# Kernel optimization log

Hardware: AMD Instinct MI355X
Metric: run time of the kernel (lower is better)

The kernel has to match this reference:

```python
import jax, jax.numpy as jnp
import numpy as np

H, W = 480, 640
N = 256
CFEAT = 256
FAR = 80.0

def _quat_to_rot(q):
    # q: [N,4] normalized (w,x,y,z)
    w, x, y, z = q[:, 0], q[:, 1], q[:, 2], q[:, 3]
    return jnp.stack([
        jnp.stack([1 - 2 * (y * y + z * z), 2 * (x * y - w * z), 2 * (x * z + w * y)], -1),
        jnp.stack([2 * (x * y + w * z), 1 - 2 * (x * x + z * z), 2 * (y * z - w * x)], -1),
        jnp.stack([2 * (x * z - w * y), 2 * (y * z + w * x), 1 - 2 * (x * x + y * y)], -1)], -2)

def setup_inputs():
    key = jax.random.key(0)
    ks = jax.random.split(key, 10)
    z = jax.random.uniform(ks[0], (N,), minval=2.0, maxval=30.0)
    x = jax.random.uniform(ks[1], (N,), minval=-0.6, maxval=0.6) * z
    y = jax.random.uniform(ks[2], (N,), minval=-0.45, maxval=0.45) * z
    means3d = jnp.stack([x, y, z], -1)                                   # [N,3] in front of camera
    features = jax.random.normal(ks[3], (N, CFEAT))                      # [N,256]
    opacities = jax.random.uniform(ks[4], (N,), minval=0.3, maxval=0.95)
    scales = jax.random.uniform(ks[5], (N, 3), minval=0.05, maxval=0.4)
    rotations = jax.random.normal(ks[6], (N, 4))                         # unnormalized quats
    cam_K = jnp.array([[500.0, 0.0, 320.0], [0.0, 500.0, 240.0], [0.0, 0.0, 1.0]])
    cam_pose = jnp.eye(4)
    w1 = jax.random.normal(ks[7], (CFEAT, 128)) * (1.0 / np.sqrt(CFEAT))
    b1 = jnp.zeros((128,))
    w2 = jax.random.normal(ks[8], (128, 128)) * (1.0 / np.sqrt(128))
    b2 = jnp.zeros((128,))
    w3 = jax.random.normal(ks[9], (128, 12)) * (1.0 / np.sqrt(128))
    b3 = jnp.zeros((12,))
    return dict(means3d=means3d, features=features, opacities=opacities, scales=scales,
                rotations=rotations, cam_K=cam_K, cam_pose=cam_pose,
                w1=w1, b1=b1, w2=w2, b2=b2, w3=w3, b3=b3)

def _render(means3d, features, opacities, scales, rotations, cam_K, cam_pose):
    fx, fy = cam_K[0, 0], cam_K[1, 1]
    cx, cy = cam_K[0, 2], cam_K[1, 2]
    Rw, tw = cam_pose[:3, :3], cam_pose[:3, 3]
    tcam = means3d @ Rw.T + tw                                           # [N,3] camera-frame
    tz = tcam[:, 2]
    valid = tz > 0.01                                                    # near_plane cull
    tzs = jnp.where(valid, tz, 1.0)
    tx, ty = tcam[:, 0], tcam[:, 1]
    # 3D covariance: Sigma = R S S^T R^T
    q = rotations / (jnp.linalg.norm(rotations, axis=1, keepdims=True) + 1e-8)
    Rq = _quat_to_rot(q)                                                 # [N,3,3]
    M = Rq * scales[:, None, :]
    Sigma = jnp.einsum('nij,nkj->nik', M, M)
    Sc = jnp.einsum('ij,njk,lk->nil', Rw, Sigma, Rw)                     # world -> camera
    # EWA projection Jacobian [N,2,3]
    zero = jnp.zeros_like(tzs)
    J = jnp.stack([
        jnp.stack([fx / tzs, zero, -fx * tx / (tzs * tzs)], -1),
        jnp.stack([zero, fy / tzs, -fy * ty / (tzs * tzs)], -1)], -2)
    cov2d = jnp.einsum('nij,njk,nlk->nil', J, Sc, J) + 0.3 * jnp.eye(2)  # low-pass dilation
    a, b, c = cov2d[:, 0, 0], cov2d[:, 0, 1], cov2d[:, 1, 1]
    inv_det = 1.0 / jnp.maximum(a * c - b * b, 1e-12)
    A, B, C = c * inv_det, -b * inv_det, a * inv_det                     # conic
    u = fx * tx / tzs + cx
    v = fy * ty / tzs + cy
    px = jnp.arange(W, dtype=jnp.float32) + 0.5
    py = jnp.arange(H, dtype=jnp.float32) + 0.5
    dx = px[None, :] - u[:, None]                                        # [N,W]
    dy = py[None, :] - v[:, None]                                        # [N,H]
    power = (-(0.5 * A)[:, None, None] * (dx * dx)[:, None, :]
             - (0.5 * C)[:, None, None] * (dy * dy)[:, :, None]
             - B[:, None, None] * dy[:, :, None] * dx[:, None, :])       # [N,H,W]
    alpha = jnp.minimum(0.99, opacities[:, None, None] * jnp.exp(jnp.minimum(power, 0.0)))
    alpha = jnp.where(valid[:, None, None] & (alpha >= 1.0 / 255.0), alpha, 0.0)
    # front-to-back alpha compositing in depth order
    order = jnp.argsort(jnp.where(valid, tz, jnp.inf))
    alpha = jnp.take(alpha, order, axis=0).reshape(N, H * W)
    feats = jnp.take(features, order, axis=0)
    tzo = jnp.take(jnp.where(valid, tz, 0.0), order, axis=0)
    T = jnp.cumprod(1.0 - alpha, axis=0)
    T_excl = jnp.concatenate([jnp.ones((1, H * W), alpha.dtype), T[:-1]], axis=0)
    wgt = T_excl * alpha                                                 # [N,P]
    feat_img = jnp.einsum('np,nc->pc', wgt, feats).reshape(H, W, CFEAT)
    depth_img = jnp.einsum('np,n->p', wgt, tzo).reshape(H, W, 1)
    return feat_img, depth_img

def reference(means3d, features, opacities, scales, rotations, cam_K, cam_pose,
              w1, b1, w2, b2, w3, b3):
    rendered, depth = _render(means3d, features, opacities, scales, rotations, cam_K, cam_pose)
    depth = jnp.clip(depth, 0.0, FAR)
    h = jax.nn.relu(rendered @ w1 + b1)
    h = jax.nn.relu(h @ w2 + b2)
    seg = (h @ w3 + b3)[None]                                            # [1,H,W,12]
    return rendered, depth, seg
```

## Files before the change

kernel.cpp:

```cpp
#include <hip/hip_runtime.h>
#include <stdint.h>

#define HH 480
#define WW 640
#define NG 256
#define CF 256
#define FARV 80.0f
#define TILES_X (WW/64)
#define AST 264
#define BST 136

typedef __attribute__((ext_vector_type(4))) float f32x4;
typedef __attribute__((ext_vector_type(8))) short s16x8;

__device__ __forceinline__ unsigned short f2bf(float f){
  union { float f; unsigned int u; } c; c.f = f;
  unsigned int u = c.u + 0x7fffu + ((c.u >> 16) & 1u);
  return (unsigned short)(u >> 16);
}
__device__ __forceinline__ float bf2f(unsigned short h){
  union { unsigned int u; float f; } c; c.u = ((unsigned int)h) << 16; return c.f;
}

__global__ __launch_bounds__(256) void k_proj(
    const float* __restrict__ means3d,
    const float* __restrict__ opac,
    const float* __restrict__ scales,
    const float* __restrict__ rots,
    const float* __restrict__ camK,
    const float* __restrict__ camP,
    float* __restrict__ wspq,
    int* __restrict__ sidx)
{
  __shared__ float keys[NG];
  const int t = threadIdx.x;

  const float fx = camK[0], fy = camK[4];
  const float cx = camK[2], cy = camK[5];
  float Rw[3][3], tw[3];
#pragma unroll
  for (int r=0;r<3;r++){
#pragma unroll
    for (int c=0;c<3;c++) Rw[r][c] = camP[r*4+c];
    tw[r] = camP[r*4+3];
  }

  float mx = means3d[t*3+0], my = means3d[t*3+1], mz = means3d[t*3+2];
  float tcx = Rw[0][0]*mx + Rw[0][1]*my + Rw[0][2]*mz + tw[0];
  float tcy = Rw[1][0]*mx + Rw[1][1]*my + Rw[1][2]*mz + tw[1];
  float tcz = Rw[2][0]*mx + Rw[2][1]*my + Rw[2][2]*mz + tw[2];
  bool valid = tcz > 0.01f;
  float tzs = valid ? tcz : 1.0f;

  float qw = rots[t*4+0], qx = rots[t*4+1];
  float qy = rots[t*4+2], qz = rots[t*4+3];
  float nrm = sqrtf(qw*qw+qx*qx+qy*qy+qz*qz) + 1e-8f;
  qw /= nrm; qx /= nrm; qy /= nrm; qz /= nrm;
  float Rq[3][3];
  {
    float xx=qx*qx, yy=qy*qy, zz=qz*qz;
    float xy=qx*qy, xz=qx*qz, yz=qy*qz;
    float wx=qw*qx, wy=qw*qy, wz=qw*qz;
    Rq[0][0]=1.f-2.f*(yy+zz); Rq[0][1]=2.f*(xy-wz); Rq[0][2]=2.f*(xz+wy);
    Rq[1][0]=2.f*(xy+wz); Rq[1][1]=1.f-2.f*(xx+zz); Rq[1][2]=2.f*(yz-wx);
    Rq[2][0]=2.f*(xz-wy); Rq[2][1]=2.f*(yz+wx); Rq[2][2]=1.f-2.f*(xx+yy);
  }
  float s0 = scales[t*3+0], s1 = scales[t*3+1], s2 = scales[t*3+2];
  float s0s=s0*s0, s1s=s1*s1, s2s=s2*s2;
  float Sig[3][3];
#pragma unroll
  for (int i=0;i<3;i++)
#pragma unroll
    for (int j=0;j<3;j++)
      Sig[i][j] = s0s*Rq[i][0]*Rq[j][0] + s1s*Rq[i][1]*Rq[j][1] + s2s*Rq[i][2]*Rq[j][2];
  float Tm[3][3];
#pragma unroll
  for (int i=0;i<3;i++)
#pragma unroll
    for (int k=0;k<3;k++)
      Tm[i][k] = Rw[i][0]*Sig[0][k] + Rw[i][1]*Sig[1][k] + Rw[i][2]*Sig[2][k];
  float Sc[3][3];
#pragma unroll
  for (int i=0;i<3;i++)
#pragma unroll
    for (int l=0;l<3;l++)
      Sc[i][l] = Tm[i][0]*Rw[l][0] + Tm[i][1]*Rw[l][1] + Tm[i][2]*Rw[l][2];

  float iz = 1.0f / tzs;
  float r00 = fx*iz, r02 = -fx*tcx*iz*iz;
  float r11 = fy*iz, r12 = -fy*tcy*iz*iz;
  float v0 = Sc[0][0]*r00 + Sc[2][0]*r02;
  float v2 = Sc[0][2]*r00 + Sc[2][2]*r02;
  float v1 = Sc[0][1]*r00 + Sc[2][1]*r02;
  float a  = r00*v0 + r02*v2 + 0.3f;
  float bb = r11*v1 + r12*v2;
  float cc = r11*(Sc[1][1]*r11 + Sc[1][2]*r12) + r12*(Sc[2][1]*r11 + Sc[2][2]*r12) + 0.3f;
  float det = a*cc - bb*bb;
  float inv_det = 1.0f / fmaxf(det, 1e-12f);
  float Av = cc*inv_det, Bv = -bb*inv_det, Cv = a*inv_det;
  float u = fx*tcx*iz + cx;
  float v = fy*tcy*iz + cy;
  float op = opac[t];
  float op_eff = valid ? op : 0.0f;
  float tzo = valid ? tcz : 0.0f;
  float rx = -1.0f, ry = -1.0f;
  if (op_eff > (1.0f/255.0f)){
    float tau = logf(255.0f*op_eff);
    if (tau > 0.0f){
      rx = sqrtf(2.0f*tau*a) + 0.5f;
      ry = sqrtf(2.0f*tau*cc) + 0.5f;
    }
  }
  float key = valid ? tcz : __builtin_inff();

  keys[t] = key;
  __syncthreads();
  int rank = 0;
  for (int j=0;j<NG;j++){
    float kj = keys[j];
    rank += (kj < key) || (kj == key && j < t);
  }
  float4* wq = (float4*)wspq;
  float4 q0; q0.x = u;       q0.y = v;  q0.z = rx;       q0.w = ry;
  float4 q1; q1.x = 0.5f*Av; q1.y = Bv; q1.z = 0.5f*Cv;  q1.w = op_eff;
  float4 q2; q2.x = tzo;     q2.y = 0.f; q2.z = 0.f;     q2.w = 0.f;
  wq[rank*3+0] = q0;
  wq[rank*3+1] = q1;
  wq[rank*3+2] = q2;
  sidx[rank] = t;
}

__global__ __launch_bounds__(256) void k_gather(
    const float* __restrict__ features,
    const float* __restrict__ w1,
    const float* __restrict__ w2,
    const float* __restrict__ w3,
    const int* __restrict__ sidx,
    unsigned short* __restrict__ wsf,
    unsigned short* __restrict__ wt1,
    unsigned short* __restrict__ wt2,
    unsigned short* __restrict__ wt3)
{
  const int bx = blockIdx.x, t = threadIdx.x;
  if (bx < 64){
    int c = bx*256 + t;
    int row = c >> 6, c4 = c & 63;
    int src = sidx[row];
    float4 f = ((const float4*)features)[src*(CF/4) + c4];
    unsigned int* dst = (unsigned int*)(wsf + row*CF + c4*4);
    dst[0] = (unsigned)f2bf(f.x) | ((unsigned)f2bf(f.y) << 16);
    dst[1] = (unsigned)f2bf(f.z) | ((unsigned)f2bf(f.w) << 16);
  } else if (bx < 96){
    int base = (bx-64)*1024 + t*4;
#pragma unroll
    for (int e=0;e<4;e++){
      int d = base + e;
      int j = d >> 8, k = d & 255;
      wt1[d] = f2bf(w1[k*128 + j]);
    }
  } else if (bx < 104){
    int base = (bx-96)*2048 + t*8;
#pragma unroll
    for (int e=0;e<8;e++){
      int d = base + e;
      int j = d >> 7, k = d & 127;
      wt2[d] = f2bf(w2[k*128 + j]);
    }
  } else {
    int base = t*8;
#pragma unroll
    for (int e=0;e<8;e++){
      int d = base + e;
      int j = d >> 7, k = d & 127;
      wt3[d] = (j < 12) ? f2bf(w3[k*12 + j]) : (unsigned short)0;
    }
  }
}

__global__ __launch_bounds__(256) void k_fused(
    const float* __restrict__ wspq,
    const unsigned short* __restrict__ wsf,
    const unsigned short* __restrict__ wt1,
    const unsigned short* __restrict__ wt2,
    const unsigned short* __restrict__ wt3,
    const float* __restrict__ b1,
    const float* __restrict__ b2,
    const float* __restrict__ b3,
    float* __restrict__ out,
    float* __restrict__ dep,
    float* __restrict__ seg)
{
  __shared__ __align__(16) unsigned char smem[64*AST*2 + 17408 + 1296];
  unsigned short* sh_A = (unsigned short*)smem;
  unsigned char* X = smem + 64*AST*2;
  float* c_u    = (float*)X;
  float* c_v    = c_u + 256;
  float* c_hA   = c_u + 512;
  float* c_Bq   = c_u + 768;
  float* c_hC   = c_u + 1024;
  float* c_op   = c_u + 1280;
  float* c_tz   = c_u + 1536;
  float* chprod = c_u + 1792;
  unsigned short* stage = (unsigned short*)X;
  unsigned short* sh_B  = (unsigned short*)X;
  unsigned char* tail = smem + 64*AST*2 + 17408;
  float* depch = (float*)tail;
  unsigned char* act_idx = tail + 1024;
  int* wcnt = (int*)(tail + 1280);

  const int t = threadIdx.x;
  const int lane = t & 63;
  const int wvi = t >> 6;
  const int y  = blockIdx.x / TILES_X;
  const int x0 = (blockIdx.x % TILES_X) * 64;

  act_idx[t] = 0;
  const float4* wq = (const float4*)wspq;
  float4 q0 = wq[t*3+0];
  bool pred = (q0.z > 0.0f)
      && (q0.x + q0.z >= (float)x0 + 0.5f)
      && (q0.x - q0.z <= (float)x0 + 63.5f)
      && (fabsf(q0.y - ((float)y + 0.5f)) <= q0.w);
  unsigned long long m = __ballot(pred);
  if (lane == 0) wcnt[wvi] = __popcll(m);
  __syncthreads();
  int base = 0;
#pragma unroll
  for (int i=0;i<4;i++) base += (i < wvi) ? wcnt[i] : 0;
  const int nact = wcnt[0]+wcnt[1]+wcnt[2]+wcnt[3];
  if (pred){
    int pos = base + __popcll(m & ((1ull << lane) - 1ull));
    float4 q1 = wq[t*3+1];
    float4 q2 = wq[t*3+2];
    act_idx[pos] = (unsigned char)t;
    c_u[pos]  = q0.x;  c_v[pos]  = q0.y;
    c_hA[pos] = q1.x;  c_Bq[pos] = q1.y;  c_hC[pos] = q1.z;
    c_op[pos] = q1.w;  c_tz[pos] = q2.x;
  }
  __syncthreads();

  const int per8 = ((((nact + 3) >> 2) + 7) & ~7);
  const int n0 = wvi * per8;
  const int n1 = (nact < n0 + per8) ? nact : (n0 + per8);
  const float px = (float)(x0 + lane) + 0.5f;
  const float py = (float)y + 0.5f;

  const int ln  = lane & 15;
  const int kq8 = (lane >> 4) * 8;
  const int rq  = (lane >> 4) * 4;
  const int cb0 = wvi * 64;
  const int la = lane & 7, lb = lane >> 3;
  const int kchunks = (nact + 31) >> 5;

  uint4 cur[4], nxt[4];
  if (kchunks > 0){
#pragma unroll
    for (int g=0; g<4; g++){
      int kk = lb + 8*g;
      cur[g] = *(const uint4*)(wsf + (int)act_idx[kk]*CF + cb0 + la*8);
    }
  }

  {
    float prod = 1.0f;
    for (int ng = n0; ng < n0 + per8; ng += 8){
      union { unsigned short s[8]; uint4 v4; } alp;
#pragma unroll
      for (int e=0;e<8;e++){
        int n = ng + e;
        float al = 0.0f;
        if (n < n1){
          float dx = px - c_u[n], dy = py - c_v[n];
          float q = c_hA[n]*dx*dx + c_Bq[n]*dx*dy + c_hC[n]*dy*dy;
          al = fminf(0.99f, c_op[n]*__expf(fminf(-q, 0.0f)));
          if (al < (1.0f/255.0f)) al = 0.0f;
        }
        alp.s[e] = f2bf(al);
        prod *= 1.0f - bf2f(alp.s[e]);
      }
      *((uint4*)&sh_A[lane*AST + ng]) = alp.v4;
    }
    chprod[t] = prod;
  }
  __syncthreads();

  {
    float T = 1.0f;
#pragma unroll
    for (int c=0;c<4;c++) if (c < wvi) T *= chprod[c*64 + lane];
    float dacc = 0.0f;
    for (int ng = n0; ng < n0 + per8; ng += 8){
      union { unsigned short s[8]; uint4 v4; } ap, wp;
      ap.v4 = *((const uint4*)&sh_A[lane*AST + ng]);
#pragma unroll
      for (int e=0;e<8;e++){
        float al = bf2f(ap.s[e]);
        float wgt = T * al;
        T *= 1.0f - al;
        wp.s[e] = f2bf(wgt);
        int n = ng + e;
        if (n < n1) dacc += wgt * c_tz[n];
      }
      *((uint4*)&sh_A[lane*AST + ng]) = wp.v4;
    }
    depch[t] = dacc;
  }
  __syncthreads();

  unsigned short* stW = stage + wvi*2048;
  const int xw = (la & 3) << 3;

  f32x4 acc[4][4];
#pragma unroll
  for (int mt=0;mt<4;mt++)
#pragma unroll
    for (int nt=0;nt<4;nt++){
      f32x4 z = {0.f,0.f,0.f,0.f};
      acc[mt][nt] = z;
    }
  for (int kb=0; kb<kchunks; kb++){
#pragma unroll
    for (int g=0; g<4; g++){
      const unsigned short* s = (const unsigned short*)&cur[g];
      int colw = (lb + 8*g) ^ xw;
#pragma unroll
      for (int i=0;i<8;i++)
        stW[(la*8 + i)*32 + colw] = s[i];
    }
    if (kb+1 < kchunks){
#pragma unroll
      for (int g=0; g<4; g++){
        int kk = (kb+1)*32 + lb + 8*g;
        nxt[g] = *(const uint4*)(wsf + (int)act_idx[kk]*CF + cb0 + la*8);
      }
    }
    int k0 = kb*32;
    s16x8 bfr[4];
#pragma unroll
    for (int nt=0;nt<4;nt++){
      int chl = nt*16 + ln;
      int colr = kq8 ^ (((chl >> 3) & 3) << 3);
      bfr[nt] = *(const s16x8*)(stW + chl*32 + colr);
    }
#pragma unroll
    for (int mt=0;mt<4;mt++){
      s16x8 afr = *(const s16x8*)(&sh_A[(mt*16 + ln)*AST + k0 + kq8]);
#pragma unroll
      for (int nt=0;nt<4;nt++)
        acc[mt][nt] = __builtin_amdgcn_mfma_f32_16x16x32_bf16(afr, bfr[nt], acc[mt][nt], 0, 0, 0);
    }
    if (kb+1 < kchunks){
#pragma unroll
      for (int g=0; g<4; g++) cur[g] = nxt[g];
    }
  }
  __syncthreads();

  if (wvi == 0){
    float d = depch[lane] + depch[64+lane] + depch[128+lane] + depch[192+lane];
    dep[y*WW + x0 + lane] = fminf(fmaxf(d, 0.0f), FARV);
  }
  const size_t Pbase = (size_t)(y*WW + x0);
#pragma unroll
  for (int mt=0;mt<4;mt++)
#pragma unroll
    for (int nt=0;nt<4;nt++)
#pragma unroll
      for (int r=0;r<4;r++){
        int row = mt*16 + rq + r;
        int col = cb0 + nt*16 + ln;
        sh_A[row*AST + col] = f2bf(acc[mt][nt][r]);
      }
  __syncthreads();

  {
    const int pxb = wvi*16;
    for (int i=0;i<16;i++){
      int pix = pxb + i;
      uint2 dv = *(const uint2*)(&sh_A[pix*AST + lane*4]);
      f32x4 o;
      o[0] = bf2f((unsigned short)(dv.x & 0xffffu));
      o[1] = bf2f((unsigned short)(dv.x >> 16));
      o[2] = bf2f((unsigned short)(dv.y & 0xffffu));
      o[3] = bf2f((unsigned short)(dv.y >> 16));
      __builtin_nontemporal_store(o, (f32x4*)(&out[(Pbase + pix)*CF + lane*4]));
    }
  }

  const int n0m = wvi * 32;
  f32x4 acc1[4][2];
#pragma unroll
  for (int nn=0;nn<2;nn++){
    float bv = b1[n0m + nn*16 + ln];
    f32x4 b4 = {bv,bv,bv,bv};
#pragma unroll
    for (int mt=0;mt<4;mt++) acc1[mt][nn] = b4;
  }
#pragma unroll
  for (int k0=0;k0<256;k0+=32){
    s16x8 bfr0 = *(const s16x8*)(wt1 + (n0m + 0*16 + ln)*256 + k0 + kq8);
    s16x8 bfr1 = *(const s16x8*)(wt1 + (n0m + 1*16 + ln)*256 + k0 + kq8);
#pragma unroll
    for (int mt=0;mt<4;mt++){
      s16x8 afr = *(const s16x8*)(&sh_A[(mt*16 + ln)*AST + k0 + kq8]);
      acc1[mt][0] = __builtin_amdgcn_mfma_f32_16x16x32_bf16(afr, bfr0, acc1[mt][0], 0, 0, 0);
      acc1[mt][1] = __builtin_amdgcn_mfma_f32_16x16x32_bf16(afr, bfr1, acc1[mt][1], 0, 0, 0);
    }
  }
  __syncthreads();
#pragma unroll
  for (int mt=0;mt<4;mt++)
#pragma unroll
    for (int nn=0;nn<2;nn++)
#pragma unroll
      for (int r=0;r<4;r++){
        int mrow = mt*16 + rq + r;
        int ncol = n0m + nn*16 + ln;
        sh_B[mrow*BST + ncol] = f2bf(fmaxf(acc1[mt][nn][r], 0.0f));
      }
  __syncthreads();

  f32x4 acc2[4][2];
#pragma unroll
  for (int nn=0;nn<2;nn++){
    float bv = b2[n0m + nn*16 + ln];
    f32x4 b4 = {bv,bv,bv,bv};
#pragma unroll
    for (int mt=0;mt<4;mt++) acc2[mt][nn] = b4;
  }
#pragma unroll
  for (int k0=0;k0<128;k0+=32){
    s16x8 bfr0 = *(const s16x8*)(wt2 + (n0m + 0*16 + ln)*128 + k0 + kq8);
    s16x8 bfr1 = *(const s16x8*)(wt2 + (n0m + 1*16 + ln)*128 + k0 + kq8);
#pragma unroll
    for (int mt=0;mt<4;mt++){
      s16x8 afr = *(const s16x8*)(&sh_B[(mt*16 + ln)*BST + k0 + kq8]);
      acc2[mt][0] = __builtin_amdgcn_mfma_f32_16x16x32_bf16(afr, bfr0, acc2[mt][0], 0, 0, 0);
      acc2[mt][1] = __builtin_amdgcn_mfma_f32_16x16x32_bf16(afr, bfr1, acc2[mt][1], 0, 0, 0);
    }
  }
  __syncthreads();
#pragma unroll
  for (int mt=0;mt<4;mt++)
#pragma unroll
    for (int nn=0;nn<2;nn++)
#pragma unroll
      for (int r=0;r<4;r++){
        int mrow = mt*16 + rq + r;
        int ncol = n0m + nn*16 + ln;
        sh_A[mrow*BST + ncol] = f2bf(fmaxf(acc2[mt][nn][r], 0.0f));
      }
  __syncthreads();

  f32x4 acc3;
  {
    float bv = (ln < 12) ? b3[ln] : 0.0f;
    f32x4 b4 = {bv,bv,bv,bv};
    acc3 = b4;
  }
#pragma unroll
  for (int k0=0;k0<128;k0+=32){
    s16x8 afr = *(const s16x8*)(&sh_A[(wvi*16 + ln)*BST + k0 + kq8]);
    s16x8 bfr = *(const s16x8*)(wt3 + ln*128 + k0 + kq8);
    acc3 = __builtin_amdgcn_mfma_f32_16x16x32_bf16(afr, bfr, acc3, 0, 0, 0);
  }
  if (ln < 12){
#pragma unroll
    for (int r=0;r<4;r++){
      int mrow = wvi*16 + rq + r;
      seg[(Pbase + mrow)*12 + ln] = acc3[r];
    }
  }
}

extern "C" void kernel_launch(void* const* d_in, const int* in_sizes, int n_in,
                              void* d_out, int out_size, void* d_ws, size_t ws_size,
                              hipStream_t stream) {
  (void)in_sizes; (void)n_in; (void)out_size; (void)ws_size;
  const float* means3d  = (const float*)d_in[0];
  const float* features = (const float*)d_in[1];
  const float* opac     = (const float*)d_in[2];
  const float* scales   = (const float*)d_in[3];
  const float* rots     = (const float*)d_in[4];
  const float* camK     = (const float*)d_in[5];
  const float* camP     = (const float*)d_in[6];
  const float* w1       = (const float*)d_in[7];
  const float* b1       = (const float*)d_in[8];
  const float* w2       = (const float*)d_in[9];
  const float* b2       = (const float*)d_in[10];
  const float* w3       = (const float*)d_in[11];
  const float* b3       = (const float*)d_in[12];

  char* ws = (char*)d_ws;
  float*          wspq = (float*)ws;
  int*            sidx = (int*)(ws + 12288);
  unsigned short* wsf  = (unsigned short*)(ws + 13312);
  unsigned short* wt1  = (unsigned short*)(ws + 144384);
  unsigned short* wt2  = (unsigned short*)(ws + 209920);
  unsigned short* wt3  = (unsigned short*)(ws + 242688);

  float* out = (float*)d_out;
  float* dep = out + (size_t)HH*WW*CF;
  float* seg = dep + (size_t)HH*WW;

  k_proj<<<1, 256, 0, stream>>>(means3d, opac, scales, rots, camK, camP, wspq, sidx);
  k_gather<<<105, 256, 0, stream>>>(features, w1, w2, w3, sidx, wsf, wt1, wt2, wt3);
  k_fused<<<HH*TILES_X, 256, 0, stream>>>(wspq, wsf, wt1, wt2, wt3, b1, b2, b3, out, dep, seg);
}
```

Measured before the change: 114.0 us.

## Shrink LDS footprint of fused kernel to fit four blocks per CU

Cuts the fused kernel's shared memory from about 52 KB to about 40 KB so four blocks can be resident per CU, and adds a matching launch bound. To do this, the per-Gaussian parameter arrays are no longer cached in LDS; they are read from global memory through the active-index list, relying on caches. The feature staging buffer is shrunk to a per-channel-tile layout, and the staging of B fragments is interleaved with the MFMA loop. The MLP hidden buffer now reuses sh_A. The trade-off is more global and cache traffic in the alpha loop, plus extra barriers, in exchange for higher occupancy.

```diff
diff --git a/kernel.cpp b/kernel.cpp
--- a/kernel.cpp
+++ b/kernel.cpp
@@ -177,7 +177,7 @@
   }
 }
 
-__global__ __launch_bounds__(256) void k_fused(
+__global__ __launch_bounds__(256, 4) void k_fused(
     const float* __restrict__ wspq,
     const unsigned short* __restrict__ wsf,
     const unsigned short* __restrict__ wt1,
@@ -190,23 +190,13 @@
     float* __restrict__ dep,
     float* __restrict__ seg)
 {
-  __shared__ __align__(16) unsigned char smem[64*AST*2 + 17408 + 1296];
-  unsigned short* sh_A = (unsigned short*)smem;
-  unsigned char* X = smem + 64*AST*2;
-  float* c_u    = (float*)X;
-  float* c_v    = c_u + 256;
-  float* c_hA   = c_u + 512;
-  float* c_Bq   = c_u + 768;
-  float* c_hC   = c_u + 1024;
-  float* c_op   = c_u + 1280;
-  float* c_tz   = c_u + 1536;
-  float* chprod = c_u + 1792;
-  unsigned short* stage = (unsigned short*)X;
-  unsigned short* sh_B  = (unsigned short*)X;
-  unsigned char* tail = smem + 64*AST*2 + 17408;
-  float* depch = (float*)tail;
-  unsigned char* act_idx = tail + 1024;
-  int* wcnt = (int*)(tail + 1280);
+  __shared__ __align__(16) unsigned char smem[40208];
+  unsigned short* sh_A  = (unsigned short*)smem;
+  unsigned short* stage = (unsigned short*)(smem + 33792);
+  float* chprod = (float*)(smem + 38912);
+  unsigned char* act_idx = smem + 39936;
+  int* wcnt = (int*)(smem + 40192);
+  float* depch = chprod;
 
   const int t = threadIdx.x;
   const int lane = t & 63;
@@ -230,12 +220,7 @@
   const int nact = wcnt[0]+wcnt[1]+wcnt[2]+wcnt[3];
   if (pred){
     int pos = base + __popcll(m & ((1ull << lane) - 1ull));
-    float4 q1 = wq[t*3+1];
-    float4 q2 = wq[t*3+2];
     act_idx[pos] = (unsigned char)t;
-    c_u[pos]  = q0.x;  c_v[pos]  = q0.y;
-    c_hA[pos] = q1.x;  c_Bq[pos] = q1.y;  c_hC[pos] = q1.z;
-    c_op[pos] = q1.w;  c_tz[pos] = q2.x;
   }
   __syncthreads();
 
@@ -249,16 +234,14 @@
   const int kq8 = (lane >> 4) * 8;
   const int rq  = (lane >> 4) * 4;
   const int cb0 = wvi * 64;
-  const int la = lane & 7, lb = lane >> 3;
+  const int la2 = lane & 1, kk = lane >> 1;
   const int kchunks = (nact + 31) >> 5;
 
   uint4 cur[4], nxt[4];
   if (kchunks > 0){
 #pragma unroll
-    for (int g=0; g<4; g++){
-      int kk = lb + 8*g;
-      cur[g] = *(const uint4*)(wsf + (int)act_idx[kk]*CF + cb0 + la*8);
-    }
+    for (int nt=0; nt<4; nt++)
+      cur[nt] = *(const uint4*)(wsf + (int)act_idx[kk]*CF + cb0 + nt*16 + la2*8);
   }
 
   {
@@ -270,9 +253,12 @@
         int n = ng + e;
         float al = 0.0f;
         if (n < n1){
-          float dx = px - c_u[n], dy = py - c_v[n];
-          float q = c_hA[n]*dx*dx + c_Bq[n]*dx*dy + c_hC[n]*dy*dy;
-          al = fminf(0.99f, c_op[n]*__expf(fminf(-q, 0.0f)));
+          int g = (int)act_idx[n];
+          float4 g0 = wq[g*3+0];
+          float4 g1 = wq[g*3+1];
+          float dx = px - g0.x, dy = py - g0.y;
+          float q = g1.x*dx*dx + g1.y*dx*dy + g1.z*dy*dy;
+          al = fminf(0.99f, g1.w*__expf(fminf(-q, 0.0f)));
           if (al < (1.0f/255.0f)) al = 0.0f;
         }
         alp.s[e] = f2bf(al);
@@ -288,6 +274,7 @@
     float T = 1.0f;
 #pragma unroll
     for (int c=0;c<4;c++) if (c < wvi) T *= chprod[c*64 + lane];
+    __syncthreads();
     float dacc = 0.0f;
     for (int ng = n0; ng < n0 + per8; ng += 8){
       union { unsigned short s[8]; uint4 v4; } ap, wp;
@@ -299,7 +286,7 @@
         T *= 1.0f - al;
         wp.s[e] = f2bf(wgt);
         int n = ng + e;
-        if (n < n1) dacc += wgt * c_tz[n];
+        if (n < n1) dacc += wgt * wspq[(int)act_idx[n]*12 + 8];
       }
       *((uint4*)&sh_A[lane*AST + ng]) = wp.v4;
     }
@@ -307,8 +294,7 @@
   }
   __syncthreads();
 
-  unsigned short* stW = stage + wvi*2048;
-  const int xw = (la & 3) << 3;
+  unsigned short* stW = stage + wvi*640;
 
   f32x4 acc[4][4];
 #pragma unroll
@@ -319,48 +305,29 @@
       acc[mt][nt] = z;
     }
   for (int kb=0; kb<kchunks; kb++){
-#pragma unroll
-    for (int g=0; g<4; g++){
-      const unsigned short* s = (const unsigned short*)&cur[g];
-      int colw = (lb + 8*g) ^ xw;
+    int k0 = kb*32;
+#pragma unroll
+    for (int nt=0;nt<4;nt++){
+      const unsigned short* s = (const unsigned short*)&cur[nt];
 #pragma unroll
       for (int i=0;i<8;i++)
-        stW[(la*8 + i)*32 + colw] = s[i];
+        stW[(la2*8 + i)*40 + kk] = s[i];
+      if (kb+1 < kchunks)
+        nxt[nt] = *(const uint4*)(wsf + (int)act_idx[(kb+1)*32 + kk]*CF + cb0 + nt*16 + la2*8);
+      s16x8 bfr = *(const s16x8*)(stW + ln*40 + kq8);
+#pragma unroll
+      for (int mt=0;mt<4;mt++){
+        s16x8 afr = *(const s16x8*)(&sh_A[(mt*16 + ln)*AST + k0 + kq8]);
+        acc[mt][nt] = __builtin_amdgcn_mfma_f32_16x16x32_bf16(afr, bfr, acc[mt][nt], 0, 0, 0);
+      }
     }
     if (kb+1 < kchunks){
 #pragma unroll
-      for (int g=0; g<4; g++){
-        int kk = (kb+1)*32 + lb + 8*g;
-        nxt[g] = *(const uint4*)(wsf + (int)act_idx[kk]*CF + cb0 + la*8);
-      }
-    }
-    int k0 = kb*32;
-    s16x8 bfr[4];
-#pragma unroll
-    for (int nt=0;nt<4;nt++){
-      int chl = nt*16 + ln;
-      int colr = kq8 ^ (((chl >> 3) & 3) << 3);
-      bfr[nt] = *(const s16x8*)(stW + chl*32 + colr);
-    }
-#pragma unroll
-    for (int mt=0;mt<4;mt++){
-      s16x8 afr = *(const s16x8*)(&sh_A[(mt*16 + ln)*AST + k0 + kq8]);
-#pragma unroll
-      for (int nt=0;nt<4;nt++)
-        acc[mt][nt] = __builtin_amdgcn_mfma_f32_16x16x32_bf16(afr, bfr[nt], acc[mt][nt], 0, 0, 0);
-    }
-    if (kb+1 < kchunks){
-#pragma unroll
-      for (int g=0; g<4; g++) cur[g] = nxt[g];
-    }
-  }
-  __syncthreads();
-
-  if (wvi == 0){
-    float d = depch[lane] + depch[64+lane] + depch[128+lane] + depch[192+lane];
-    dep[y*WW + x0 + lane] = fminf(fmaxf(d, 0.0f), FARV);
-  }
-  const size_t Pbase = (size_t)(y*WW + x0);
+      for (int nt=0;nt<4;nt++) cur[nt] = nxt[nt];
+    }
+  }
+  __syncthreads();
+
 #pragma unroll
   for (int mt=0;mt<4;mt++)
 #pragma unroll
@@ -372,6 +339,8 @@
         sh_A[row*AST + col] = f2bf(acc[mt][nt][r]);
       }
   __syncthreads();
+
+  const size_t Pbase = (size_t)(y*WW + x0);
 
   {
     const int pxb = wvi*16;
@@ -386,6 +355,10 @@
       __builtin_nontemporal_store(o, (f32x4*)(&out[(Pbase + pix)*CF + lane*4]));
     }
   }
+  if (wvi == 0){
+    float d = depch[lane] + depch[64+lane] + depch[128+lane] + depch[192+lane];
+    dep[y*WW + x0 + lane] = fminf(fmaxf(d, 0.0f), FARV);
+  }
 
   const int n0m = wvi * 32;
   f32x4 acc1[4][2];
@@ -416,7 +389,7 @@
       for (int r=0;r<4;r++){
         int mrow = mt*16 + rq + r;
         int ncol = n0m + nn*16 + ln;
-        sh_B[mrow*BST + ncol] = f2bf(fmaxf(acc1[mt][nn][r], 0.0f));
+        sh_A[mrow*BST + ncol] = f2bf(fmaxf(acc1[mt][nn][r], 0.0f));
       }
   __syncthreads();
 
@@ -434,7 +407,7 @@
     s16x8 bfr1 = *(const s16x8*)(wt2 + (n0m + 1*16 + ln)*128 + k0 + kq8);
 #pragma unroll
     for (int mt=0;mt<4;mt++){
-      s16x8 afr = *(const s16x8*)(&sh_B[(mt*16 + ln)*BST + k0 + kq8]);
+      s16x8 afr = *(const s16x8*)(&sh_A[(mt*16 + ln)*BST + k0 + kq8]);
       acc2[mt][0] = __builtin_amdgcn_mfma_f32_16x16x32_bf16(afr, bfr0, acc2[mt][0], 0, 0, 0);
       acc2[mt][1] = __builtin_amdgcn_mfma_f32_16x16x32_bf16(afr, bfr1, acc2[mt][1], 0, 0, 0);
     }
```

Result: slower. 119.7 us (+5.0%).
